# Optimization experiments

Measured on AMD Instinct MI355X. Metric: run time of the kernel, lower is better.

The kernel has to match this reference:

```python
import jax, jax.numpy as jnp
import numpy as np

N = 4096      # total_activities_num
D = 128       # feature dim
E = 1_000_000 # number of edges (events)
EPS = 1e-12


def setup_inputs() -> dict:
    key = jax.random.key(0)
    k1, k2, k3, k4, k5 = jax.random.split(key, 5)
    currents = jax.random.randint(k1, (E,), 0, N, dtype=jnp.int64)
    targets = jax.random.randint(k2, (E,), 0, N, dtype=jnp.int64)
    activities_features = jax.random.normal(k3, (N, D), dtype=jnp.float32)
    cases_features = jax.random.normal(k4, (E, D), dtype=jnp.float32)
    # Learned parameter W [N, N], kaiming_uniform fan_in relu -> U(-b, b), b = sqrt(6/fan_in)
    bound = float(np.sqrt(6.0 / N))
    W = jax.random.uniform(k5, (N, N), dtype=jnp.float32, minval=-bound, maxval=bound)
    return {
        "currents": currents,
        "targets": targets,
        "activities_features": activities_features,
        "cases_features": cases_features,
        "W": W,
    }


def reference(currents, targets, activities_features, cases_features, W):
    # Per-edge gather: h_emb, t_emb are [E, D]
    h_emb = activities_features[currents]
    t_emb = activities_features[targets]
    # dist = ||h + case - t||_2 per edge -> [E]
    diff = h_emb + cases_features - t_emb
    dist = jnp.sqrt(jnp.sum(diff * diff, axis=1))
    vals = jnp.exp(-dist)
    # Scatter-add into dense [N, N] attention input at (tail, head)
    att_input = jnp.zeros((N, N), dtype=activities_features.dtype)
    att_input = att_input.at[targets, currents].add(vals)
    # Row-normalize
    norm = jnp.sum(att_input, axis=1, keepdims=True)
    attention = att_input / (norm + EPS)
    # Dense GEMMs
    feat = W @ activities_features           # [N, D]
    h = attention @ feat + feat               # [N, D]
    return h
```

## Files before the change

kernel.cpp:

```cpp
#include <hip/hip_runtime.h>
#include <hip/hip_bf16.h>

typedef unsigned short u16;
typedef unsigned int   u32;

typedef __attribute__((ext_vector_type(8))) __bf16 bf16x8;
typedef __attribute__((ext_vector_type(4))) float  f32x4;
typedef __attribute__((ext_vector_type(4))) u32    u32x4;

#define NN 4096
#define DD 128
#define EPS 1e-12f

#define KS 4
#define BM 32
#define BK 128
#define KPER (NN / KS)
#define LDK 136

static __device__ __forceinline__ u16 f2bf(float f) {
    union { float f; u32 u; } v; v.f = f;
    u32 r = v.u + 0x7fffu + ((v.u >> 16) & 1u);
    return (u16)(r >> 16);
}
static __device__ __forceinline__ float bf2f(u16 u) {
    union { u32 i; float f; } v; v.i = (u32)u << 16; return v.f;
}

template <typename T>
static __device__ __forceinline__ auto bf2_atomic_add(T* p, T v, int)
    -> decltype(unsafeAtomicAdd(p, v), void()) {
    unsafeAtomicAdd(p, v);
}
template <typename T>
static __device__ __forceinline__ void bf2_atomic_add(T* p, T v, long) {
    u32* w = (u32*)p;
    union { u32 i; T h; } av; av.h = v;
    float alo = bf2f((u16)(av.i & 0xffff));
    float ahi = bf2f((u16)(av.i >> 16));
    u32 old = *w, assumed;
    do {
        assumed = old;
        float lo = bf2f((u16)(assumed & 0xffff)) + alo;
        float hi = bf2f((u16)(assumed >> 16)) + ahi;
        u32 nv = (u32)f2bf(lo) | ((u32)f2bf(hi) << 16);
        old = atomicCAS(w, assumed, nv);
    } while (old != assumed);
}

__global__ __launch_bounds__(256) void edge_kernel(
    const int* __restrict__ currents, const int* __restrict__ targets,
    const float* __restrict__ A, const float* __restrict__ cases,
    u16* __restrict__ att, int E)
{
    int e = blockIdx.x * 8 + (threadIdx.x >> 5);
    if (e >= E) return;
    int l = threadIdx.x & 31;
    int c = currents[e];
    int t = targets[e];
    f32x4 h = *(const f32x4*)(A + (size_t)c * DD + l * 4);
    f32x4 g = *(const f32x4*)(A + (size_t)t * DD + l * 4);
    f32x4 q = __builtin_nontemporal_load((const f32x4*)(cases + (size_t)e * DD + l * 4));
    f32x4 d = h + q - g;
    float s = d.x * d.x + d.y * d.y + d.z * d.z + d.w * d.w;
#pragma unroll
    for (int m = 16; m; m >>= 1) s += __shfl_xor(s, m, 64);
    if (l == 0) {
        float val = __expf(-__fsqrt_rn(s));
        u16 b = f2bf(val);
        size_t off = (size_t)t * NN + c;
        union { u32 i; __hip_bfloat162 h2; } pk;
        pk.i = (c & 1) ? ((u32)b << 16) : (u32)b;
        bf2_atomic_add((__hip_bfloat162*)(att + (off & ~(size_t)1)), pk.h2, 0);
    }
}

__global__ __launch_bounds__(256) void transpose_to_bf16(
    const float* __restrict__ in, u16* __restrict__ out)
{
    __shared__ __align__(16) u16 lds[128][40];
    const int k0 = blockIdx.x * 32;
    const int t = threadIdx.x;
#pragma unroll
    for (int i = 0; i < 4; ++i) {
        int f  = t + 256 * i;
        int kr = f >> 5;
        int n0 = (f & 31) * 4;
        float4 v = *(const float4*)(in + (size_t)(k0 + kr) * DD + n0);
        lds[n0 + 0][kr] = f2bf(v.x);
        lds[n0 + 1][kr] = f2bf(v.y);
        lds[n0 + 2][kr] = f2bf(v.z);
        lds[n0 + 3][kr] = f2bf(v.w);
    }
    __syncthreads();
    int n = t >> 1, h = t & 1;
    uint4 v0 = *(const uint4*)&lds[n][h * 16];
    uint4 v1 = *(const uint4*)&lds[n][h * 16 + 8];
    *(uint4*)(out + (size_t)n * NN + k0 + h * 16)     = v0;
    *(uint4*)(out + (size_t)n * NN + k0 + h * 16 + 8) = v1;
}

template<bool ROWSUM, bool ABF16>
__global__ __launch_bounds__(512, 4) void gemm_splitk(
    const void* __restrict__ AmatV,
    const u16*  __restrict__ BT,
    float* __restrict__ part,
    float* __restrict__ rsum_part)
{
    __shared__ __align__(16) u16 As[BM * LDK];
    __shared__ __align__(16) u16 Bs[DD * LDK];

    const int m0   = blockIdx.x * BM;
    const int ks   = blockIdx.y;
    const int kbeg = ks * KPER;
    const int t    = threadIdx.x;
    const int wave = t >> 6;
    const int lane = t & 63;
    const int quad = lane >> 4;
    const int l16  = lane & 15;

    const int ar = t >> 4;
    const int aq = t & 15;
    const int bn = t >> 2;
    const int bq = t & 3;

    const float* Apf = (const float*)AmatV + (size_t)(m0 + ar) * NN + kbeg + aq * 4;
    const u16*   Aph = (const u16*)AmatV   + (size_t)(m0 + ar) * NN + kbeg + aq * 8;
    const u16*   Bp  = BT + (size_t)bn * NN + kbeg + bq * 32;

    f32x4 vaA0, vaA1, vaB0, vaB1; u32x4 vahA, vahB;
    if constexpr (ABF16) {
        vahA = __builtin_nontemporal_load((const u32x4*)Aph);
        vahB = __builtin_nontemporal_load((const u32x4*)(Aph + BK));
    } else {
        vaA0 = __builtin_nontemporal_load((const f32x4*)Apf);
        vaA1 = __builtin_nontemporal_load((const f32x4*)(Apf + 64));
        vaB0 = __builtin_nontemporal_load((const f32x4*)(Apf + BK));
        vaB1 = __builtin_nontemporal_load((const f32x4*)(Apf + BK + 64));
    }
    uint4 vb0 = *(const uint4*)(Bp);
    uint4 vb1 = *(const uint4*)(Bp + 8);
    uint4 vb2 = *(const uint4*)(Bp + 16);
    uint4 vb3 = *(const uint4*)(Bp + 24);

    f32x4 acc0 = {0.f, 0.f, 0.f, 0.f};
    f32x4 acc1 = {0.f, 0.f, 0.f, 0.f};
    float rsum = 0.f;

#define STAGE_A_BF16(VAH)                                                   \
    {                                                                       \
        if (ROWSUM) {                                                       \
            _Pragma("unroll")                                               \
            for (int j = 0; j < 4; ++j) {                                   \
                u32 w = (VAH)[j];                                           \
                rsum += bf2f((u16)(w & 0xffff)) + bf2f((u16)(w >> 16));     \
            }                                                               \
        }                                                                   \
        *(u32x4*)&As[ar * LDK + aq * 8] = (VAH);                            \
    }
#define STAGE_A_F32(V0, V1)                                                 \
    {                                                                       \
        if (ROWSUM) {                                                       \
            rsum += ((V0).x + (V0).y) + ((V0).z + (V0).w)                   \
                  + ((V1).x + (V1).y) + ((V1).z + (V1).w);                  \
        }                                                                   \
        ushort4 u0, u1;                                                     \
        u0.x = f2bf((V0).x); u0.y = f2bf((V0).y);                           \
        u0.z = f2bf((V0).z); u0.w = f2bf((V0).w);                           \
        u1.x = f2bf((V1).x); u1.y = f2bf((V1).y);                           \
        u1.z = f2bf((V1).z); u1.w = f2bf((V1).w);                           \
        *(ushort4*)&As[ar * LDK + aq * 4]      = u0;                        \
        *(ushort4*)&As[ar * LDK + aq * 4 + 64] = u1;                        \
    }
#define STAGE_B()                                                           \
    {                                                                       \
        *(uint4*)&Bs[bn * LDK + bq * 32]      = vb0;                        \
        *(uint4*)&Bs[bn * LDK + bq * 32 + 8]  = vb1;                        \
        *(uint4*)&Bs[bn * LDK + bq * 32 + 16] = vb2;                        \
        *(uint4*)&Bs[bn * LDK + bq * 32 + 24] = vb3;                        \
    }
#define LOAD_B(KOFF)                                                        \
    {                                                                       \
        vb0 = *(const uint4*)(Bp + (KOFF));                                 \
        vb1 = *(const uint4*)(Bp + (KOFF) + 8);                             \
        vb2 = *(const uint4*)(Bp + (KOFF) + 16);                            \
        vb3 = *(const uint4*)(Bp + (KOFF) + 24);                            \
    }
#define MFMA_PHASE()                                                        \
    _Pragma("unroll")                                                       \
    for (int k2 = 0; k2 < 4; ++k2) {                                        \
        bf16x8 a0 = *(const bf16x8*)&As[l16 * LDK + k2 * 32 + quad * 8];    \
        bf16x8 a1 = *(const bf16x8*)&As[(16 + l16) * LDK + k2 * 32 + quad * 8]; \
        bf16x8 b  = *(const bf16x8*)&Bs[(wave * 16 + l16) * LDK + k2 * 32 + quad * 8]; \
        acc0 = __builtin_amdgcn_mfma_f32_16x16x32_bf16(a0, b, acc0, 0, 0, 0); \
        acc1 = __builtin_amdgcn_mfma_f32_16x16x32_bf16(a1, b, acc1, 0, 0, 0); \
    }

    for (int kk = 0; kk < KPER; kk += 2 * BK) {
        if constexpr (ABF16) { STAGE_A_BF16(vahA); } else { STAGE_A_F32(vaA0, vaA1); }
        STAGE_B();
        __syncthreads();
        if (kk + 2 * BK < KPER) {
            if constexpr (ABF16) {
                vahA = __builtin_nontemporal_load((const u32x4*)(Aph + kk + 2 * BK));
            } else {
                vaA0 = __builtin_nontemporal_load((const f32x4*)(Apf + kk + 2 * BK));
                vaA1 = __builtin_nontemporal_load((const f32x4*)(Apf + kk + 2 * BK + 64));
            }
        }
        LOAD_B(kk + BK);
        MFMA_PHASE();
        __syncthreads();

        if constexpr (ABF16) { STAGE_A_BF16(vahB); } else { STAGE_A_F32(vaB0, vaB1); }
        STAGE_B();
        __syncthreads();
        if (kk + 3 * BK < KPER) {
            if constexpr (ABF16) {
                vahB = __builtin_nontemporal_load((const u32x4*)(Aph + kk + 3 * BK));
            } else {
                vaB0 = __builtin_nontemporal_load((const f32x4*)(Apf + kk + 3 * BK));
                vaB1 = __builtin_nontemporal_load((const f32x4*)(Apf + kk + 3 * BK + 64));
            }
        }
        if (kk + 2 * BK < KPER) LOAD_B(kk + 2 * BK);
        MFMA_PHASE();
        __syncthreads();
    }

    float* P = part + (size_t)ks * NN * DD;
#pragma unroll
    for (int r = 0; r < 4; ++r) {
        int row0 = m0 + quad * 4 + r;
        int col  = wave * 16 + l16;
        P[(size_t)row0 * DD + col]        = acc0[r];
        P[(size_t)(row0 + 16) * DD + col] = acc1[r];
    }

    if (ROWSUM) {
#pragma unroll
        for (int m = 8; m; m >>= 1) rsum += __shfl_xor(rsum, m, 64);
        if ((t & 15) == 0) rsum_part[ks * NN + m0 + ar] = rsum;
    }
#undef STAGE_A_BF16
#undef STAGE_A_F32
#undef STAGE_B
#undef LOAD_B
#undef MFMA_PHASE
}

__global__ __launch_bounds__(256) void combine_feat_bt2(
    const float* __restrict__ part, float* __restrict__ feat,
    u16* __restrict__ BT2)
{
    __shared__ __align__(16) u16 lt[128][40];
    const int b = blockIdx.x;
    const int t = threadIdx.x;
    const int S = NN * DD / 4;
    const int base = b * 1024;
#pragma unroll
    for (int it = 0; it < 4; ++it) {
        int i = base + it * 256 + t;
        const float4* p = (const float4*)part;
        float4 a = p[i], b4 = p[i + S], c = p[i + 2 * S], d = p[i + 3 * S];
        float4 s;
        s.x = (a.x + b4.x) + (c.x + d.x);
        s.y = (a.y + b4.y) + (c.y + d.y);
        s.z = (a.z + b4.z) + (c.z + d.z);
        s.w = (a.w + b4.w) + (c.w + d.w);
        ((float4*)feat)[i] = s;
        int lrow = it * 8 + (t >> 5);
        int col0 = (i & 31) * 4;
        lt[col0 + 0][lrow] = f2bf(s.x);
        lt[col0 + 1][lrow] = f2bf(s.y);
        lt[col0 + 2][lrow] = f2bf(s.z);
        lt[col0 + 3][lrow] = f2bf(s.w);
    }
    __syncthreads();
    int col = t >> 1, half = t & 1;
    uint4 v0 = *(const uint4*)&lt[col][half * 16];
    uint4 v1 = *(const uint4*)&lt[col][half * 16 + 8];
    *(uint4*)(BT2 + (size_t)col * NN + b * 32 + half * 16)     = v0;
    *(uint4*)(BT2 + (size_t)col * NN + b * 32 + half * 16 + 8) = v1;
}

__global__ __launch_bounds__(256) void combine_out(
    const float* __restrict__ part, const float* __restrict__ rsum_part,
    const float* __restrict__ feat, float* __restrict__ out)
{
    int i = blockIdx.x * 256 + threadIdx.x;
    int row = i >> 5;
    const float4* p = (const float4*)part;
    const int S = NN * DD / 4;
    float4 a = p[i], b = p[i + S], c = p[i + 2 * S], d = p[i + 3 * S];
    float ns = (rsum_part[row] + rsum_part[row + NN])
             + (rsum_part[row + 2 * NN] + rsum_part[row + 3 * NN]);
    float sc = 1.0f / (ns + EPS);
    float4 f = ((const float4*)feat)[i];
    float4 s;
    s.x = ((a.x + b.x) + (c.x + d.x)) * sc + f.x;
    s.y = ((a.y + b.y) + (c.y + d.y)) * sc + f.y;
    s.z = ((a.z + b.z) + (c.z + d.z)) * sc + f.z;
    s.w = ((a.w + b.w) + (c.w + d.w)) * sc + f.w;
    ((float4*)out)[i] = s;
}

extern "C" void kernel_launch(void* const* d_in, const int* in_sizes, int n_in,
                              void* d_out, int out_size, void* d_ws, size_t ws_size,
                              hipStream_t stream)
{
    const int*   currents = (const int*)d_in[0];
    const int*   targets  = (const int*)d_in[1];
    const float* acts     = (const float*)d_in[2];
    const float* cases    = (const float*)d_in[3];
    const float* W        = (const float*)d_in[4];
    float*       out      = (float*)d_out;
    const int E = in_sizes[0];

    char* ws = (char*)d_ws;
    u16*   att       = (u16*)ws;
    float* part      = (float*)(ws + (size_t)NN * NN * 2);
    float* feat      = part + (size_t)KS * NN * DD;
    u16*   BT1       = (u16*)(feat + (size_t)NN * DD);
    u16*   BT2       = BT1 + (size_t)DD * NN;
    float* rsum_part = (float*)(BT2 + (size_t)DD * NN);

    hipMemsetAsync(att, 0, (size_t)NN * NN * 2, stream);

    transpose_to_bf16<<<128, 256, 0, stream>>>(acts, BT1);

    edge_kernel<<<(E + 7) / 8, 256, 0, stream>>>(currents, targets, acts, cases,
                                                 att, E);

    gemm_splitk<false, false><<<dim3(NN / BM, KS), 512, 0, stream>>>(W, BT1, part, nullptr);
    combine_feat_bt2<<<128, 256, 0, stream>>>(part, feat, BT2);

    gemm_splitk<true, true><<<dim3(NN / BM, KS), 512, 0, stream>>>(att, BT2, part, rsum_part);
    combine_out<<<NN * DD / 4 / 256, 256, 0, stream>>>(part, rsum_part, feat, out);
}
```

Measured before the change: 189.9 us.

## Replace split-K GEMMs with full-K BM=16 GEMMs fusing epilogues and memset

Drops the split-K scheme (4 partial buffers plus combine kernels) and has each block compute a 16-row tile over the full K range. The epilogue writes feat and the transposed bf16 copy directly, or applies the row normalization and residual add in place. The att memset is folded into the transpose prep kernel as extra zeroing blocks. This removes two combine kernels, the partial-sum traffic and a memset launch, at the cost of fewer blocks (256 instead of 512) with longer serial K loops and one MFMA per phase instead of two.

```diff
diff --git a/kernel.cpp b/kernel.cpp
--- a/kernel.cpp
+++ b/kernel.cpp
@@ -6,17 +6,16 @@
 
 typedef __attribute__((ext_vector_type(8))) __bf16 bf16x8;
 typedef __attribute__((ext_vector_type(4))) float  f32x4;
-typedef __attribute__((ext_vector_type(4))) u32    u32x4;
+typedef __attribute__((ext_vector_type(2))) u32    u32x2;
 
 #define NN 4096
 #define DD 128
 #define EPS 1e-12f
 
-#define KS 4
-#define BM 32
+#define BM 16
 #define BK 128
-#define KPER (NN / KS)
 #define LDK 136
+#define NZERO 2048
 
 static __device__ __forceinline__ u16 f2bf(float f) {
     union { float f; u32 u; } v; v.f = f;
@@ -48,6 +47,39 @@
     } while (old != assumed);
 }
 
+__global__ __launch_bounds__(256) void prep_kernel(
+    const float* __restrict__ in, u16* __restrict__ out, uint4* __restrict__ attz)
+{
+    __shared__ __align__(16) u16 lds[128][40];
+    const int t = threadIdx.x;
+    if (blockIdx.x >= 128) {
+        const size_t b = blockIdx.x - 128;
+        uint4 z = make_uint4(0u, 0u, 0u, 0u);
+#pragma unroll
+        for (int i = 0; i < 4; ++i)
+            attz[b * 1024 + i * 256 + t] = z;
+        return;
+    }
+    const int k0 = blockIdx.x * 32;
+#pragma unroll
+    for (int i = 0; i < 4; ++i) {
+        int f  = t + 256 * i;
+        int kr = f >> 5;
+        int n0 = (f & 31) * 4;
+        float4 v = *(const float4*)(in + (size_t)(k0 + kr) * DD + n0);
+        lds[n0 + 0][kr] = f2bf(v.x);
+        lds[n0 + 1][kr] = f2bf(v.y);
+        lds[n0 + 2][kr] = f2bf(v.z);
+        lds[n0 + 3][kr] = f2bf(v.w);
+    }
+    __syncthreads();
+    int n = t >> 1, h = t & 1;
+    uint4 v0 = *(const uint4*)&lds[n][h * 16];
+    uint4 v1 = *(const uint4*)&lds[n][h * 16 + 8];
+    *(uint4*)(out + (size_t)n * NN + k0 + h * 16)     = v0;
+    *(uint4*)(out + (size_t)n * NN + k0 + h * 16 + 8) = v1;
+}
+
 __global__ __launch_bounds__(256) void edge_kernel(
     const int* __restrict__ currents, const int* __restrict__ targets,
     const float* __restrict__ A, const float* __restrict__ cases,
@@ -75,102 +107,62 @@
     }
 }
 
-__global__ __launch_bounds__(256) void transpose_to_bf16(
-    const float* __restrict__ in, u16* __restrict__ out)
-{
-    __shared__ __align__(16) u16 lds[128][40];
-    const int k0 = blockIdx.x * 32;
-    const int t = threadIdx.x;
-#pragma unroll
-    for (int i = 0; i < 4; ++i) {
-        int f  = t + 256 * i;
-        int kr = f >> 5;
-        int n0 = (f & 31) * 4;
-        float4 v = *(const float4*)(in + (size_t)(k0 + kr) * DD + n0);
-        lds[n0 + 0][kr] = f2bf(v.x);
-        lds[n0 + 1][kr] = f2bf(v.y);
-        lds[n0 + 2][kr] = f2bf(v.z);
-        lds[n0 + 3][kr] = f2bf(v.w);
-    }
-    __syncthreads();
-    int n = t >> 1, h = t & 1;
-    uint4 v0 = *(const uint4*)&lds[n][h * 16];
-    uint4 v1 = *(const uint4*)&lds[n][h * 16 + 8];
-    *(uint4*)(out + (size_t)n * NN + k0 + h * 16)     = v0;
-    *(uint4*)(out + (size_t)n * NN + k0 + h * 16 + 8) = v1;
-}
-
-template<bool ROWSUM, bool ABF16>
-__global__ __launch_bounds__(512, 4) void gemm_splitk(
+template<bool G2>
+__global__ __launch_bounds__(512, 4) void gemm_fused(
     const void* __restrict__ AmatV,
     const u16*  __restrict__ BT,
-    float* __restrict__ part,
-    float* __restrict__ rsum_part)
+    float* __restrict__ feat,
+    u16*   __restrict__ BT2,
+    float* __restrict__ outp)
 {
     __shared__ __align__(16) u16 As[BM * LDK];
     __shared__ __align__(16) u16 Bs[DD * LDK];
 
     const int m0   = blockIdx.x * BM;
-    const int ks   = blockIdx.y;
-    const int kbeg = ks * KPER;
     const int t    = threadIdx.x;
     const int wave = t >> 6;
     const int lane = t & 63;
     const int quad = lane >> 4;
     const int l16  = lane & 15;
 
-    const int ar = t >> 4;
-    const int aq = t & 15;
+    const int ar = t >> 5;
+    const int aq = t & 31;
     const int bn = t >> 2;
     const int bq = t & 3;
 
-    const float* Apf = (const float*)AmatV + (size_t)(m0 + ar) * NN + kbeg + aq * 4;
-    const u16*   Aph = (const u16*)AmatV   + (size_t)(m0 + ar) * NN + kbeg + aq * 8;
-    const u16*   Bp  = BT + (size_t)bn * NN + kbeg + bq * 32;
-
-    f32x4 vaA0, vaA1, vaB0, vaB1; u32x4 vahA, vahB;
-    if constexpr (ABF16) {
-        vahA = __builtin_nontemporal_load((const u32x4*)Aph);
-        vahB = __builtin_nontemporal_load((const u32x4*)(Aph + BK));
+    const float* Apf = (const float*)AmatV + (size_t)(m0 + ar) * NN + aq * 4;
+    const u16*   Aph = (const u16*)AmatV   + (size_t)(m0 + ar) * NN + aq * 4;
+    const u16*   Bp  = BT + (size_t)bn * NN + bq * 32;
+
+    f32x4 vaA, vaB; u32x2 vahA, vahB;
+    if constexpr (G2) {
+        vahA = __builtin_nontemporal_load((const u32x2*)Aph);
+        vahB = __builtin_nontemporal_load((const u32x2*)(Aph + BK));
     } else {
-        vaA0 = __builtin_nontemporal_load((const f32x4*)Apf);
-        vaA1 = __builtin_nontemporal_load((const f32x4*)(Apf + 64));
-        vaB0 = __builtin_nontemporal_load((const f32x4*)(Apf + BK));
-        vaB1 = __builtin_nontemporal_load((const f32x4*)(Apf + BK + 64));
+        vaA = __builtin_nontemporal_load((const f32x4*)Apf);
+        vaB = __builtin_nontemporal_load((const f32x4*)(Apf + BK));
     }
     uint4 vb0 = *(const uint4*)(Bp);
     uint4 vb1 = *(const uint4*)(Bp + 8);
     uint4 vb2 = *(const uint4*)(Bp + 16);
     uint4 vb3 = *(const uint4*)(Bp + 24);
 
-    f32x4 acc0 = {0.f, 0.f, 0.f, 0.f};
-    f32x4 acc1 = {0.f, 0.f, 0.f, 0.f};
+    f32x4 acc = {0.f, 0.f, 0.f, 0.f};
     float rsum = 0.f;
 
 #define STAGE_A_BF16(VAH)                                                   \
     {                                                                       \
-        if (ROWSUM) {                                                       \
-            _Pragma("unroll")                                               \
-            for (int j = 0; j < 4; ++j) {                                   \
-                u32 w = (VAH)[j];                                           \
-                rsum += bf2f((u16)(w & 0xffff)) + bf2f((u16)(w >> 16));     \
-            }                                                               \
-        }                                                                   \
-        *(u32x4*)&As[ar * LDK + aq * 8] = (VAH);                            \
-    }
-#define STAGE_A_F32(V0, V1)                                                 \
-    {                                                                       \
-        if (ROWSUM) {                                                       \
-            rsum += ((V0).x + (V0).y) + ((V0).z + (V0).w)                   \
-                  + ((V1).x + (V1).y) + ((V1).z + (V1).w);                  \
-        }                                                                   \
-        ushort4 u0, u1;                                                     \
-        u0.x = f2bf((V0).x); u0.y = f2bf((V0).y);                           \
-        u0.z = f2bf((V0).z); u0.w = f2bf((V0).w);                           \
-        u1.x = f2bf((V1).x); u1.y = f2bf((V1).y);                           \
-        u1.z = f2bf((V1).z); u1.w = f2bf((V1).w);                           \
-        *(ushort4*)&As[ar * LDK + aq * 4]      = u0;                        \
-        *(ushort4*)&As[ar * LDK + aq * 4 + 64] = u1;                        \
+        u32 w0 = (VAH)[0], w1 = (VAH)[1];                                   \
+        rsum += (bf2f((u16)(w0 & 0xffff)) + bf2f((u16)(w0 >> 16)))          \
+              + (bf2f((u16)(w1 & 0xffff)) + bf2f((u16)(w1 >> 16)));         \
+        *(u32x2*)&As[ar * LDK + aq * 4] = (VAH);                            \
+    }
+#define STAGE_A_F32(V)                                                      \
+    {                                                                       \
+        ushort4 u;                                                          \
+        u.x = f2bf((V).x); u.y = f2bf((V).y);                               \
+        u.z = f2bf((V).z); u.w = f2bf((V).w);                               \
+        *(ushort4*)&As[ar * LDK + aq * 4] = u;                              \
     }
 #define STAGE_B()                                                           \
     {                                                                       \
@@ -189,120 +181,72 @@
 #define MFMA_PHASE()                                                        \
     _Pragma("unroll")                                                       \
     for (int k2 = 0; k2 < 4; ++k2) {                                        \
-        bf16x8 a0 = *(const bf16x8*)&As[l16 * LDK + k2 * 32 + quad * 8];    \
-        bf16x8 a1 = *(const bf16x8*)&As[(16 + l16) * LDK + k2 * 32 + quad * 8]; \
-        bf16x8 b  = *(const bf16x8*)&Bs[(wave * 16 + l16) * LDK + k2 * 32 + quad * 8]; \
-        acc0 = __builtin_amdgcn_mfma_f32_16x16x32_bf16(a0, b, acc0, 0, 0, 0); \
-        acc1 = __builtin_amdgcn_mfma_f32_16x16x32_bf16(a1, b, acc1, 0, 0, 0); \
-    }
-
-    for (int kk = 0; kk < KPER; kk += 2 * BK) {
-        if constexpr (ABF16) { STAGE_A_BF16(vahA); } else { STAGE_A_F32(vaA0, vaA1); }
+        bf16x8 a = *(const bf16x8*)&As[l16 * LDK + k2 * 32 + quad * 8];     \
+        bf16x8 b = *(const bf16x8*)&Bs[(wave * 16 + l16) * LDK + k2 * 32 + quad * 8]; \
+        acc = __builtin_amdgcn_mfma_f32_16x16x32_bf16(a, b, acc, 0, 0, 0);  \
+    }
+
+    for (int kk = 0; kk < NN; kk += 2 * BK) {
+        if constexpr (G2) { STAGE_A_BF16(vahA); } else { STAGE_A_F32(vaA); }
         STAGE_B();
         __syncthreads();
-        if (kk + 2 * BK < KPER) {
-            if constexpr (ABF16) {
-                vahA = __builtin_nontemporal_load((const u32x4*)(Aph + kk + 2 * BK));
+        if (kk + 2 * BK < NN) {
+            if constexpr (G2) {
+                vahA = __builtin_nontemporal_load((const u32x2*)(Aph + kk + 2 * BK));
             } else {
-                vaA0 = __builtin_nontemporal_load((const f32x4*)(Apf + kk + 2 * BK));
-                vaA1 = __builtin_nontemporal_load((const f32x4*)(Apf + kk + 2 * BK + 64));
+                vaA = __builtin_nontemporal_load((const f32x4*)(Apf + kk + 2 * BK));
             }
         }
         LOAD_B(kk + BK);
         MFMA_PHASE();
         __syncthreads();
 
-        if constexpr (ABF16) { STAGE_A_BF16(vahB); } else { STAGE_A_F32(vaB0, vaB1); }
+        if constexpr (G2) { STAGE_A_BF16(vahB); } else { STAGE_A_F32(vaB); }
         STAGE_B();
         __syncthreads();
-        if (kk + 3 * BK < KPER) {
-            if constexpr (ABF16) {
-                vahB = __builtin_nontemporal_load((const u32x4*)(Aph + kk + 3 * BK));
+        if (kk + 3 * BK < NN) {
+            if constexpr (G2) {
+                vahB = __builtin_nontemporal_load((const u32x2*)(Aph + kk + 3 * BK));
             } else {
-                vaB0 = __builtin_nontemporal_load((const f32x4*)(Apf + kk + 3 * BK));
-                vaB1 = __builtin_nontemporal_load((const f32x4*)(Apf + kk + 3 * BK + 64));
+                vaB = __builtin_nontemporal_load((const f32x4*)(Apf + kk + 3 * BK));
             }
         }
-        if (kk + 2 * BK < KPER) LOAD_B(kk + 2 * BK);
+        if (kk + 2 * BK < NN) LOAD_B(kk + 2 * BK);
         MFMA_PHASE();
         __syncthreads();
     }
 
-    float* P = part + (size_t)ks * NN * DD;
-#pragma unroll
-    for (int r = 0; r < 4; ++r) {
-        int row0 = m0 + quad * 4 + r;
-        int col  = wave * 16 + l16;
-        P[(size_t)row0 * DD + col]        = acc0[r];
-        P[(size_t)(row0 + 16) * DD + col] = acc1[r];
-    }
-
-    if (ROWSUM) {
-#pragma unroll
-        for (int m = 8; m; m >>= 1) rsum += __shfl_xor(rsum, m, 64);
-        if ((t & 15) == 0) rsum_part[ks * NN + m0 + ar] = rsum;
+    const int col = wave * 16 + l16;
+    if constexpr (!G2) {
+#pragma unroll
+        for (int r = 0; r < 4; ++r)
+            feat[(size_t)(m0 + quad * 4 + r) * DD + col] = acc[r];
+        u16* lt = (u16*)Bs;
+#pragma unroll
+        for (int r = 0; r < 4; ++r)
+            lt[col * 24 + quad * 4 + r] = f2bf(acc[r]);
+        __syncthreads();
+        int c2 = t & 127, seg = t >> 7;
+        u32x2 v = *(const u32x2*)&lt[c2 * 24 + seg * 4];
+        *(u32x2*)(BT2 + (size_t)c2 * NN + m0 + seg * 4) = v;
+    } else {
+#pragma unroll
+        for (int m = 16; m; m >>= 1) rsum += __shfl_xor(rsum, m, 64);
+        float* scs = (float*)As;
+        if ((t & 31) == 0) scs[ar] = 1.0f / (rsum + EPS);
+        __syncthreads();
+#pragma unroll
+        for (int r = 0; r < 4; ++r) {
+            int row = quad * 4 + r;
+            outp[(size_t)(m0 + row) * DD + col] =
+                acc[r] * scs[row] + feat[(size_t)(m0 + row) * DD + col];
+        }
     }
 #undef STAGE_A_BF16
 #undef STAGE_A_F32
 #undef STAGE_B
 #undef LOAD_B
 #undef MFMA_PHASE
-}
-
-__global__ __launch_bounds__(256) void combine_feat_bt2(
-    const float* __restrict__ part, float* __restrict__ feat,
-    u16* __restrict__ BT2)
-{
-    __shared__ __align__(16) u16 lt[128][40];
-    const int b = blockIdx.x;
-    const int t = threadIdx.x;
-    const int S = NN * DD / 4;
-    const int base = b * 1024;
-#pragma unroll
-    for (int it = 0; it < 4; ++it) {
-        int i = base + it * 256 + t;
-        const float4* p = (const float4*)part;
-        float4 a = p[i], b4 = p[i + S], c = p[i + 2 * S], d = p[i + 3 * S];
-        float4 s;
-        s.x = (a.x + b4.x) + (c.x + d.x);
-        s.y = (a.y + b4.y) + (c.y + d.y);
-        s.z = (a.z + b4.z) + (c.z + d.z);
-        s.w = (a.w + b4.w) + (c.w + d.w);
-        ((float4*)feat)[i] = s;
-        int lrow = it * 8 + (t >> 5);
-        int col0 = (i & 31) * 4;
-        lt[col0 + 0][lrow] = f2bf(s.x);
-        lt[col0 + 1][lrow] = f2bf(s.y);
-        lt[col0 + 2][lrow] = f2bf(s.z);
-        lt[col0 + 3][lrow] = f2bf(s.w);
-    }
-    __syncthreads();
-    int col = t >> 1, half = t & 1;
-    uint4 v0 = *(const uint4*)&lt[col][half * 16];
-    uint4 v1 = *(const uint4*)&lt[col][half * 16 + 8];
-    *(uint4*)(BT2 + (size_t)col * NN + b * 32 + half * 16)     = v0;
-    *(uint4*)(BT2 + (size_t)col * NN + b * 32 + half * 16 + 8) = v1;
-}
-
-__global__ __launch_bounds__(256) void combine_out(
-    const float* __restrict__ part, const float* __restrict__ rsum_part,
-    const float* __restrict__ feat, float* __restrict__ out)
-{
-    int i = blockIdx.x * 256 + threadIdx.x;
-    int row = i >> 5;
-    const float4* p = (const float4*)part;
-    const int S = NN * DD / 4;
-    float4 a = p[i], b = p[i + S], c = p[i + 2 * S], d = p[i + 3 * S];
-    float ns = (rsum_part[row] + rsum_part[row + NN])
-             + (rsum_part[row + 2 * NN] + rsum_part[row + 3 * NN]);
-    float sc = 1.0f / (ns + EPS);
-    float4 f = ((const float4*)feat)[i];
-    float4 s;
-    s.x = ((a.x + b.x) + (c.x + d.x)) * sc + f.x;
-    s.y = ((a.y + b.y) + (c.y + d.y)) * sc + f.y;
-    s.z = ((a.z + b.z) + (c.z + d.z)) * sc + f.z;
-    s.w = ((a.w + b.w) + (c.w + d.w)) * sc + f.w;
-    ((float4*)out)[i] = s;
 }
 
 extern "C" void kernel_launch(void* const* d_in, const int* in_sizes, int n_in,
@@ -318,23 +262,17 @@
     const int E = in_sizes[0];
 
     char* ws = (char*)d_ws;
-    u16*   att       = (u16*)ws;
-    float* part      = (float*)(ws + (size_t)NN * NN * 2);
-    float* feat      = part + (size_t)KS * NN * DD;
-    u16*   BT1       = (u16*)(feat + (size_t)NN * DD);
-    u16*   BT2       = BT1 + (size_t)DD * NN;
-    float* rsum_part = (float*)(BT2 + (size_t)DD * NN);
-
-    hipMemsetAsync(att, 0, (size_t)NN * NN * 2, stream);
-
-    transpose_to_bf16<<<128, 256, 0, stream>>>(acts, BT1);
+    u16*   att  = (u16*)ws;
+    float* feat = (float*)(ws + (size_t)NN * NN * 2);
+    u16*   BT1  = (u16*)(feat + (size_t)NN * DD);
+    u16*   BT2  = BT1 + (size_t)DD * NN;
+
+    prep_kernel<<<128 + NZERO, 256, 0, stream>>>(acts, BT1, (uint4*)att);
 
     edge_kernel<<<(E + 7) / 8, 256, 0, stream>>>(currents, targets, acts, cases,
                                                  att, E);
 
-    gemm_splitk<false, false><<<dim3(NN / BM, KS), 512, 0, stream>>>(W, BT1, part, nullptr);
-    combine_feat_bt2<<<128, 256, 0, stream>>>(part, feat, BT2);
-
-    gemm_splitk<true, true><<<dim3(NN / BM, KS), 512, 0, stream>>>(att, BT2, part, rsum_part);
-    combine_out<<<NN * DD / 4 / 256, 256, 0, stream>>>(part, rsum_part, feat, out);
-}
+    gemm_fused<false><<<NN / BM, 512, 0, stream>>>(W, BT1, feat, BT2, nullptr);
+
+    gemm_fused<true><<<NN / BM, 512, 0, stream>>>(att, BT2, feat, nullptr, out);
+}
```

After: 209.8 us. 1.1x slower.
